# Kernel optimization log

Measured on AMD Instinct MI355X. Metric: run time of the kernel, lower is better.

## Reference

```python
import jax, jax.numpy as jnp
import numpy as np

B, C, H, W = 16, 128, 64, 64
C_OUT = 256
N_BANDS = 4
KS = [3, 5, 7, 11]
BN_EPS = 1e-5


def setup_inputs() -> dict:
    key = jax.random.key(0)
    ks = jax.random.split(key, 16)
    inp = {
        'x': jax.random.normal(ks[0], (B, C, H, W), dtype=jnp.float32),
        'conv_w0': jax.random.normal(ks[1], (C, 1, 3), dtype=jnp.float32) * 0.2,
        'conv_w1': jax.random.normal(ks[2], (C, 1, 5), dtype=jnp.float32) * 0.2,
        'conv_w2': jax.random.normal(ks[3], (C, 1, 7), dtype=jnp.float32) * 0.2,
        'conv_w3': jax.random.normal(ks[4], (C, 1, 11), dtype=jnp.float32) * 0.2,
        'bn_gamma': jax.random.uniform(ks[5], (N_BANDS, C), dtype=jnp.float32, minval=0.5, maxval=1.5),
        'bn_beta': jax.random.normal(ks[6], (N_BANDS, C), dtype=jnp.float32) * 0.1,
        'bn_mean': jax.random.normal(ks[7], (N_BANDS, C), dtype=jnp.float32) * 0.1,
        'bn_var': jax.random.uniform(ks[8], (N_BANDS, C), dtype=jnp.float32, minval=0.5, maxval=1.5),
        'scale_weights': jnp.ones((N_BANDS,), dtype=jnp.float32),
        'alpha': jnp.float32(0.5),
        'proj_w': jax.random.normal(ks[9], (C_OUT, C * N_BANDS), dtype=jnp.float32) * 0.04,
        'proj_b': jax.random.normal(ks[10], (C_OUT,), dtype=jnp.float32) * 0.02,
    }
    return inp


def _dwconv1d(xc, w):
    # xc: [B, C, L], w: [C, 1, k] depthwise, 'same' padding for odd k
    k = w.shape[-1]
    return jax.lax.conv_general_dilated(
        xc, w, window_strides=(1,), padding=[(k // 2, k // 2)],
        feature_group_count=xc.shape[1], dimension_numbers=('NCH', 'OIH', 'NCH'))


def _forward(x, conv_w0, conv_w1, conv_w2, conv_w3, bn_gamma, bn_beta, bn_mean,
             bn_var, scale_weights, alpha, proj_w, proj_b):
    b, c, h, w = x.shape
    L = h * w
    xs = x.reshape(b, c, L)                      # [B, C, L] (== x.view.transpose.transpose)
    norm_w = jax.nn.softmax(scale_weights)       # [n_bands]

    # --- multi-scale depthwise conv branch: conv -> BN(eval) -> GELU -> scale ---
    conv_bands = []
    for i, cw in enumerate([conv_w0, conv_w1, conv_w2, conv_w3]):
        y = _dwconv1d(xs, cw)                    # [B, C, L]
        inv = jax.lax.rsqrt(bn_var[i] + BN_EPS)  # [C]
        y = (y - bn_mean[i][:, None]) * (inv * bn_gamma[i])[:, None] + bn_beta[i][:, None]
        y = jax.nn.gelu(y, approximate=False)    # exact erf GELU (torch default)
        conv_bands.append(y.transpose(0, 2, 1) * norm_w[i])  # [B, L, C]

    # --- frequency band branch (interpolate to size L is identity: conv keeps L) ---
    xt = xs.transpose(0, 2, 1)                   # [B, L, C]
    Xf = jnp.fft.rfft(xt, axis=1)                # [B, n_freqs, C]
    n_freqs = L // 2 + 1
    band_size = n_freqs // N_BANDS
    fidx = jnp.arange(n_freqs)
    alpha_s = jax.nn.sigmoid(alpha)
    fused = []
    for i in range(N_BANDS):
        start = i * band_size
        end = (i + 1) * band_size if i < N_BANDS - 1 else n_freqs
        mask = (fidx >= start) & (fidx < end)
        band = jnp.fft.irfft(jnp.where(mask[None, :, None], Xf, 0), n=L, axis=1)
        fused.append(alpha_s * conv_bands[i] + (1.0 - alpha_s) * band)

    cat = jnp.concatenate(fused, axis=-1)        # [B, L, n_bands*C]
    out = cat @ proj_w.T + proj_b                # [B, L, C_out]
    return out.transpose(0, 2, 1).reshape(b, -1, h, w)


def reference(x, conv_w0, conv_w1, conv_w2, conv_w3, bn_gamma, bn_beta, bn_mean,
              bn_var, scale_weights, alpha, proj_w, proj_b):
    return _forward(x, conv_w0, conv_w1, conv_w2, conv_w3, bn_gamma, bn_beta,
                    bn_mean, bn_var, scale_weights, alpha, proj_w, proj_b)
```

## Files before the change

### kernel.cpp

```cpp
#include <hip/hip_runtime.h>
#include <math.h>

constexpr int LEN = 4096;
constexpr int NTHREADS = 512;
constexpr int PELEM = LEN / NTHREADS;
constexpr float INVN = 1.0f / 4096.0f;
constexpr float RHALF = 0.70710678118654752440f;
constexpr float TWK = -1.5339807878856412e-3f;

typedef __attribute__((ext_vector_type(8))) short bf16x8;
typedef __attribute__((ext_vector_type(4))) float f32x4;

#define APHYS(I) ((I) + ((I) >> 5))
#define ZOFF 8

__device__ __forceinline__ unsigned short f2bf(float f) {
    unsigned u = __float_as_uint(f);
    unsigned r = (u + 0x7fffu + ((u >> 16) & 1u)) >> 16;
    return (unsigned short)r;
}

__device__ __forceinline__ int drev3(int t) {
    return ((t & 7) << 6) | (((t >> 3) & 7) << 3) | (t >> 6);
}

__device__ __forceinline__ void cmul(float ar, float ai, float br, float bi,
                                     float& cr, float& ci) {
    cr = ar * br - ai * bi;
    ci = ar * bi + ai * br;
}

__device__ __forceinline__ void dft8_fwd(float (&xr)[8], float (&xi)[8]) {
    float b0r = xr[0] + xr[4], b0i = xi[0] + xi[4];
    float b1r = xr[1] + xr[5], b1i = xi[1] + xi[5];
    float b2r = xr[2] + xr[6], b2i = xi[2] + xi[6];
    float b3r = xr[3] + xr[7], b3i = xi[3] + xi[7];
    float c0r = xr[0] - xr[4], c0i = xi[0] - xi[4];
    float c1r = xr[1] - xr[5], c1i = xi[1] - xi[5];
    float c2r = xr[2] - xr[6], c2i = xi[2] - xi[6];
    float c3r = xr[3] - xr[7], c3i = xi[3] - xi[7];
    float d1r = RHALF * (c1r + c1i), d1i = RHALF * (c1i - c1r);
    float d2r = c2i,               d2i = -c2r;
    float d3r = -RHALF * (c3r - c3i), d3i = -RHALF * (c3r + c3i);
    float t0r = b0r + b2r, t0i = b0i + b2i;
    float t1r = b0r - b2r, t1i = b0i - b2i;
    float t2r = b1r + b3r, t2i = b1i + b3i;
    float t3r = b1r - b3r, t3i = b1i - b3i;
    xr[0] = t0r + t2r; xi[0] = t0i + t2i;
    xr[2] = t1r + t3i; xi[2] = t1i - t3r;
    xr[4] = t0r - t2r; xi[4] = t0i - t2i;
    xr[6] = t1r - t3i; xi[6] = t1i + t3r;
    t0r = c0r + d2r; t0i = c0i + d2i;
    t1r = c0r - d2r; t1i = c0i - d2i;
    t2r = d1r + d3r; t2i = d1i + d3i;
    t3r = d1r - d3r; t3i = d1i - d3i;
    xr[1] = t0r + t2r; xi[1] = t0i + t2i;
    xr[3] = t1r + t3i; xi[3] = t1i - t3r;
    xr[5] = t0r - t2r; xi[5] = t0i - t2i;
    xr[7] = t1r - t3i; xi[7] = t1i + t3r;
}

__device__ __forceinline__ void dft8_inv(float (&xr)[8], float (&xi)[8]) {
    float b0r = xr[0] + xr[4], b0i = xi[0] + xi[4];
    float b1r = xr[1] + xr[5], b1i = xi[1] + xi[5];
    float b2r = xr[2] + xr[6], b2i = xi[2] + xi[6];
    float b3r = xr[3] + xr[7], b3i = xi[3] + xi[7];
    float c0r = xr[0] - xr[4], c0i = xi[0] - xi[4];
    float c1r = xr[1] - xr[5], c1i = xi[1] - xi[5];
    float c2r = xr[2] - xr[6], c2i = xi[2] - xi[6];
    float c3r = xr[3] - xr[7], c3i = xi[3] - xi[7];
    float d1r = RHALF * (c1r - c1i), d1i = RHALF * (c1r + c1i);
    float d2r = -c2i,              d2i = c2r;
    float d3r = -RHALF * (c3r + c3i), d3i = RHALF * (c3r - c3i);
    float t0r = b0r + b2r, t0i = b0i + b2i;
    float t1r = b0r - b2r, t1i = b0i - b2i;
    float t2r = b1r + b3r, t2i = b1i + b3i;
    float t3r = b1r - b3r, t3i = b1i - b3i;
    xr[0] = t0r + t2r; xi[0] = t0i + t2i;
    xr[2] = t1r - t3i; xi[2] = t1i + t3r;
    xr[4] = t0r - t2r; xi[4] = t0i - t2i;
    xr[6] = t1r + t3i; xi[6] = t1i - t3r;
    t0r = c0r + d2r; t0i = c0i + d2i;
    t1r = c0r - d2r; t1i = c0i - d2i;
    t2r = d1r + d3r; t2i = d1i + d3i;
    t3r = d1r - d3r; t3i = d1i - d3i;
    xr[1] = t0r + t2r; xi[1] = t0i + t2i;
    xr[3] = t1r - t3i; xi[3] = t1i + t3r;
    xr[5] = t0r - t2r; xi[5] = t0i - t2i;
    xr[7] = t1r + t3i; xi[7] = t1i - t3r;
}

template <bool CONJ>
__device__ __forceinline__ void twmul7(float (&xr)[8], float (&xi)[8], int k1) {
    float sv, cv;
    __sincosf(TWK * (float)k1, &sv, &cv);
    float w1r = cv;
    float w1i = CONJ ? -sv : sv;
    float w2r, w2i, w3r, w3i, w4r, w4i, w5r, w5i, w6r, w6i, w7r, w7i;
    cmul(w1r, w1i, w1r, w1i, w2r, w2i);
    cmul(w2r, w2i, w1r, w1i, w3r, w3i);
    cmul(w2r, w2i, w2r, w2i, w4r, w4i);
    cmul(w4r, w4i, w1r, w1i, w5r, w5i);
    cmul(w4r, w4i, w2r, w2i, w6r, w6i);
    cmul(w4r, w4i, w3r, w3i, w7r, w7i);
    float orr, oii;
    cmul(xr[1], xi[1], w1r, w1i, orr, oii); xr[1] = orr; xi[1] = oii;
    cmul(xr[2], xi[2], w2r, w2i, orr, oii); xr[2] = orr; xi[2] = oii;
    cmul(xr[3], xi[3], w3r, w3i, orr, oii); xr[3] = orr; xi[3] = oii;
    cmul(xr[4], xi[4], w4r, w4i, orr, oii); xr[4] = orr; xi[4] = oii;
    cmul(xr[5], xi[5], w5r, w5i, orr, oii); xr[5] = orr; xi[5] = oii;
    cmul(xr[6], xi[6], w6r, w6i, orr, oii); xr[6] = orr; xi[6] = oii;
    cmul(xr[7], xi[7], w7r, w7i, orr, oii); xr[7] = orr; xi[7] = oii;
}

__device__ void dif_head(float* __restrict__ ar, float* __restrict__ ai, int tid) {
#pragma unroll
    for (int s = 0; s < 3; ++s) {
        __syncthreads();
        const int eshift = 3 * (3 - s);
        const int E = 1 << eshift;
        int j = tid & (E - 1);
        int g = tid >> eshift;
        int base = (g << (eshift + 3)) + j;
        float xr[8], xi[8];
#pragma unroll
        for (int m = 0; m < 8; ++m) {
            int idx = APHYS(base + (m << eshift));
            xr[m] = ar[idx]; xi[m] = ai[idx];
        }
        dft8_fwd(xr, xi);
        twmul7<false>(xr, xi, j << (3 * s));
#pragma unroll
        for (int m = 0; m < 8; ++m) {
            int idx = APHYS(base + (m << eshift));
            ar[idx] = xr[m]; ai[idx] = xi[m];
        }
    }
}

__device__ void dit_tail(float* __restrict__ ar, float* __restrict__ ai, int tid) {
#pragma unroll
    for (int s = 1; s < 4; ++s) {
        __syncthreads();
        const int eshift = 3 * s;
        const int E = 1 << eshift;
        int j = tid & (E - 1);
        int g = tid >> eshift;
        int base = (g << (eshift + 3)) + j;
        float xr[8], xi[8];
#pragma unroll
        for (int m = 0; m < 8; ++m) {
            int idx = APHYS(base + (m << eshift));
            xr[m] = ar[idx]; xi[m] = ai[idx];
        }
        twmul7<true>(xr, xi, j << (3 * (3 - s)));
        dft8_inv(xr, xi);
#pragma unroll
        for (int m = 0; m < 8; ++m) {
            int idx = APHYS(base + (m << eshift));
            ar[idx] = xr[m]; ai[idx] = xi[m];
        }
    }
}

__global__ __launch_bounds__(512) void k_bands(
    const float* __restrict__ x,
    const float* __restrict__ cw0, const float* __restrict__ cw1,
    const float* __restrict__ cw2, const float* __restrict__ cw3,
    const float* __restrict__ bng, const float* __restrict__ bnb,
    const float* __restrict__ bnm, const float* __restrict__ bnv,
    const float* __restrict__ sw, const float* __restrict__ alp,
    unsigned int* __restrict__ Fu) {
    __shared__ float wr[4223], wi[4223];
    __shared__ unsigned zpk[LEN + 16];

    const int tid = threadIdx.x;
    const int pair = blockIdx.x;
    const int b = blockIdx.y;
    const int c0 = 2 * pair, c1 = c0 + 1;

    const float* xp0 = x + ((size_t)b * 128 + c0) * LEN;
    const float* xp1 = xp0 + LEN;
#pragma unroll
    for (int p = 0; p < PELEM; ++p) {
        int l = tid + NTHREADS * p;
        float a0 = xp0[l], a1 = xp1[l];
        zpk[ZOFF + l] = (unsigned)f2bf(a0) | ((unsigned)f2bf(a1) << 16);
        wr[APHYS(l)] = a0; wi[APHYS(l)] = a1;
    }
    if (tid < 8) {
        zpk[tid] = 0u;
        zpk[ZOFF + LEN + tid] = 0u;
    }

    dif_head(wr, wi, tid);
    float Zr[8], Zi[8];
    __syncthreads();
#pragma unroll
    for (int m = 0; m < 8; ++m) {
        int idx = APHYS(8 * tid + m);
        Zr[m] = wr[idx]; Zi[m] = wi[idx];
    }
    dft8_fwd(Zr, Zi);

    const int D = drev3(tid);
    const int BM[8]  = {0, 1, 2, 3, 3, 2, 1, 0};
    const int BM0[8] = {0, 1, 2, 3, 3, 3, 2, 1};

    float s0w = sw[0], s1w = sw[1], s2w = sw[2], s3w = sw[3];
    float mx = fmaxf(fmaxf(s0w, s1w), fmaxf(s2w, s3w));
    float e0 = expf(s0w - mx), e1 = expf(s1w - mx), e2 = expf(s2w - mx), e3 = expf(s3w - mx);
    float esum = e0 + e1 + e2 + e3;
    float nwv[4] = {e0 / esum, e1 / esum, e2 / esum, e3 / esum};
    float alpha_s = 1.0f / (1.0f + expf(-alp[0]));
    float omaI = (1.0f - alpha_s) * INVN;

    const float* cwp[4] = {cw0, cw1, cw2, cw3};
    const int kk4[4] = {3, 5, 7, 11};

    unsigned int* dst = Fu + (size_t)b * (512 * LEN / 2);
    const int n = tid & 15;

#pragma unroll
    for (int band = 0; band < 4; ++band) {
        {
            float xr[8], xi[8];
#pragma unroll
            for (int m = 0; m < 8; ++m) {
                int bb = (D != 0) ? BM[m] : BM0[m];
                bool keep = (bb == band);
                xr[m] = keep ? Zr[m] : 0.0f;
                xi[m] = keep ? Zi[m] : 0.0f;
            }
            dft8_inv(xr, xi);
            __syncthreads();
#pragma unroll
            for (int m = 0; m < 8; ++m) {
                int idx = APHYS(8 * tid + m);
                wr[idx] = xr[m]; wi[idx] = xi[m];
            }
            dit_tail(wr, wi, tid);
        }

        const float* cw = cwp[band];
        const int kk = kk4[band];
        const int kh = kk >> 1;
        float A0 = rsqrtf(bnv[band * 128 + c0] + 1e-5f) * bng[band * 128 + c0];
        float B0 = bnb[band * 128 + c0] - bnm[band * 128 + c0] * A0;
        float A1 = rsqrtf(bnv[band * 128 + c1] + 1e-5f) * bng[band * 128 + c1];
        float B1 = bnb[band * 128 + c1] - bnm[band * 128 + c1] * A1;
        float nww = nwv[band];
#pragma unroll
        for (int p = 0; p < PELEM; ++p) {
            int l = tid + NTHREADS * p;
            float bvr = wr[APHYS(l)];
            float bvi = wi[APHYS(l)];
            float s0 = 0.f, s1 = 0.f;
#pragma unroll
            for (int q = 0; q < 11; ++q) {
                if (q < kk) {
                    unsigned uv = zpk[ZOFF + l + q - kh];
                    s0 += __uint_as_float(uv << 16) * cw[c0 * kk + q];
                    s1 += __uint_as_float(uv & 0xffff0000u) * cw[c1 * kk + q];
                }
            }
            float y0 = s0 * A0 + B0;
            y0 = 0.5f * y0 * (1.0f + erff(y0 * RHALF)) * nww;
            float y1 = s1 * A1 + B1;
            y1 = 0.5f * y1 * (1.0f + erff(y1 * RHALF)) * nww;
            float f0 = alpha_s * y0 + omaI * bvr;
            float f1 = alpha_s * y1 + omaI * bvi;
            int lb = (tid >> 4) + 32 * p;
            unsigned int val = (unsigned int)f2bf(f0) | ((unsigned int)f2bf(f1) << 16);
            dst[((lb * 64 + pair) * 16 + n) * 4 + band] = val;
        }
    }
}

__global__ void k_prep(const float* __restrict__ pw, unsigned short* __restrict__ Wq) {
    int idx = blockIdx.x * 256 + threadIdx.x;
    int o = idx >> 9, c = idx & 511;
    int band = c >> 7, pair = (c & 127) >> 1, lo = c & 1;
    int dstidx = (((o >> 4) * 64 + pair) * 16 + (o & 15)) * 8 + 2 * band + lo;
    Wq[dstidx] = f2bf(pw[idx]);
}

__global__ __launch_bounds__(256) void k_gemm(
    const unsigned short* __restrict__ Wq, const unsigned short* __restrict__ Fq,
    const float* __restrict__ pb, float* __restrict__ out) {
    const int tid = threadIdx.x;
    const int wave = tid >> 6, lane = tid & 63;
    const int h = lane >> 4, n16 = lane & 15;
    const int lt = blockIdx.x, b = blockIdx.y;
    const unsigned short* Fb = Fq + (size_t)b * 2097152;

    f32x4 acc[4][4];
#pragma unroll
    for (int mi = 0; mi < 4; ++mi)
#pragma unroll
        for (int ni = 0; ni < 4; ++ni) acc[mi][ni] = (f32x4){0.f, 0.f, 0.f, 0.f};

#pragma unroll
    for (int ks = 0; ks < 16; ++ks) {
        bf16x8 af[4], bfr[4];
#pragma unroll
        for (int mi = 0; mi < 4; ++mi) {
            int mb = wave * 4 + mi;
            af[mi] = *(const bf16x8*)(Wq + ((((mb * 64) + 4 * ks + h) * 16 + n16) << 3));
        }
#pragma unroll
        for (int ni = 0; ni < 4; ++ni) {
            int lb = lt * 4 + ni;
            bfr[ni] = *(const bf16x8*)(Fb + ((((lb * 64) + 4 * ks + h) * 16 + n16) << 3));
        }
#pragma unroll
        for (int mi = 0; mi < 4; ++mi)
#pragma unroll
            for (int ni = 0; ni < 4; ++ni)
                acc[mi][ni] = __builtin_amdgcn_mfma_f32_16x16x32_bf16(
                    af[mi], bfr[ni], acc[mi][ni], 0, 0, 0);
    }

#pragma unroll
    for (int mi = 0; mi < 4; ++mi) {
#pragma unroll
        for (int r = 0; r < 4; ++r) {
            int o = wave * 64 + mi * 16 + h * 4 + r;
            float bias = pb[o];
#pragma unroll
            for (int ni = 0; ni < 4; ++ni) {
                int l = lt * 64 + ni * 16 + n16;
                out[((size_t)(b * 256 + o)) * LEN + l] = acc[mi][ni][r] + bias;
            }
        }
    }
}

extern "C" void kernel_launch(void* const* d_in, const int* in_sizes, int n_in,
                              void* d_out, int out_size, void* d_ws, size_t ws_size,
                              hipStream_t stream) {
    const float* x   = (const float*)d_in[0];
    const float* cw0 = (const float*)d_in[1];
    const float* cw1 = (const float*)d_in[2];
    const float* cw2 = (const float*)d_in[3];
    const float* cw3 = (const float*)d_in[4];
    const float* bng = (const float*)d_in[5];
    const float* bnb = (const float*)d_in[6];
    const float* bnm = (const float*)d_in[7];
    const float* bnv = (const float*)d_in[8];
    const float* sw  = (const float*)d_in[9];
    const float* alp = (const float*)d_in[10];
    const float* pw  = (const float*)d_in[11];
    const float* pb  = (const float*)d_in[12];
    float* out = (float*)d_out;

    unsigned short* Wq = (unsigned short*)d_ws;
    unsigned int* Fu = (unsigned int*)((char*)d_ws + 262144);

    k_prep<<<512, 256, 0, stream>>>(pw, Wq);

    const size_t perB = (size_t)512 * LEN * 2;
    int chunk = (int)((ws_size > 262144 ? ws_size - 262144 : 0) / perB);
    if (chunk < 1) chunk = 1;
    if (chunk > 16) chunk = 16;

    for (int b0 = 0; b0 < 16; b0 += chunk) {
        int nb = 16 - b0 < chunk ? 16 - b0 : chunk;
        dim3 g1(64, nb);
        k_bands<<<g1, NTHREADS, 0, stream>>>(
            x + (size_t)b0 * 128 * LEN, cw0, cw1, cw2, cw3,
            bng, bnb, bnm, bnv, sw, alp, Fu);
        dim3 g2(64, nb);
        k_gemm<<<g2, 256, 0, stream>>>(
            Wq, (const unsigned short*)Fu, pb, out + (size_t)b0 * 256 * LEN);
    }
}
```

Baseline: 145.9 us.

## Fuse FFT first/last radix stages into registers and derive last band by subtraction

The first DIF radix-8 stage now runs directly on the values loaded from global memory, and the last DIT stage of each inverse transform stays in registers. This removes one shared-memory round trip and one barrier per transform. The fourth frequency band's inverse FFT is skipped and computed as the input minus the sum of the other three bands, since the band masks partition the spectrum. The conv input is now kept in fp32 shared arrays instead of packed bf16, which raises LDS use and may lower occupancy, but improves precision.

```diff
diff --git a/kernel.cpp b/kernel.cpp
--- a/kernel.cpp
+++ b/kernel.cpp
@@ -113,9 +113,9 @@
     cmul(xr[7], xi[7], w7r, w7i, orr, oii); xr[7] = orr; xi[7] = oii;
 }
 
-__device__ void dif_head(float* __restrict__ ar, float* __restrict__ ai, int tid) {
-#pragma unroll
-    for (int s = 0; s < 3; ++s) {
+__device__ void dif_mid(float* __restrict__ ar, float* __restrict__ ai, int tid) {
+#pragma unroll
+    for (int s = 1; s < 3; ++s) {
         __syncthreads();
         const int eshift = 3 * (3 - s);
         const int E = 1 << eshift;
@@ -138,9 +138,9 @@
     }
 }
 
-__device__ void dit_tail(float* __restrict__ ar, float* __restrict__ ai, int tid) {
-#pragma unroll
-    for (int s = 1; s < 4; ++s) {
+__device__ void dit_mid(float* __restrict__ ar, float* __restrict__ ai, int tid) {
+#pragma unroll
+    for (int s = 1; s < 3; ++s) {
         __syncthreads();
         const int eshift = 3 * s;
         const int E = 1 << eshift;
@@ -171,8 +171,8 @@
     const float* __restrict__ bnm, const float* __restrict__ bnv,
     const float* __restrict__ sw, const float* __restrict__ alp,
     unsigned int* __restrict__ Fu) {
+    __shared__ float zr[LEN + 16], zi[LEN + 16];
     __shared__ float wr[4223], wi[4223];
-    __shared__ unsigned zpk[LEN + 16];
 
     const int tid = threadIdx.x;
     const int pair = blockIdx.x;
@@ -181,21 +181,31 @@
 
     const float* xp0 = x + ((size_t)b * 128 + c0) * LEN;
     const float* xp1 = xp0 + LEN;
+
+    float Ar[8], Ai[8];
 #pragma unroll
     for (int p = 0; p < PELEM; ++p) {
         int l = tid + NTHREADS * p;
         float a0 = xp0[l], a1 = xp1[l];
-        zpk[ZOFF + l] = (unsigned)f2bf(a0) | ((unsigned)f2bf(a1) << 16);
-        wr[APHYS(l)] = a0; wi[APHYS(l)] = a1;
+        zr[ZOFF + l] = a0; zi[ZOFF + l] = a1;
+        Ar[p] = a0; Ai[p] = a1;
     }
     if (tid < 8) {
-        zpk[tid] = 0u;
-        zpk[ZOFF + LEN + tid] = 0u;
-    }
-
-    dif_head(wr, wi, tid);
+        zr[tid] = 0.f; zi[tid] = 0.f;
+        zr[ZOFF + LEN + tid] = 0.f; zi[ZOFF + LEN + tid] = 0.f;
+    }
+
+    dft8_fwd(Ar, Ai);
+    twmul7<false>(Ar, Ai, tid);
+#pragma unroll
+    for (int m = 0; m < 8; ++m) {
+        int idx = APHYS(tid + (m << 9));
+        wr[idx] = Ar[m]; wi[idx] = Ai[m];
+    }
+    dif_mid(wr, wi, tid);
+
+    __syncthreads();
     float Zr[8], Zi[8];
-    __syncthreads();
 #pragma unroll
     for (int m = 0; m < 8; ++m) {
         int idx = APHYS(8 * tid + m);
@@ -213,17 +223,22 @@
     float esum = e0 + e1 + e2 + e3;
     float nwv[4] = {e0 / esum, e1 / esum, e2 / esum, e3 / esum};
     float alpha_s = 1.0f / (1.0f + expf(-alp[0]));
-    float omaI = (1.0f - alpha_s) * INVN;
+    float oma = 1.0f - alpha_s;
 
     const float* cwp[4] = {cw0, cw1, cw2, cw3};
     const int kk4[4] = {3, 5, 7, 11};
 
+    float accr[PELEM], acci[PELEM];
+#pragma unroll
+    for (int p = 0; p < PELEM; ++p) { accr[p] = 0.f; acci[p] = 0.f; }
+
     unsigned int* dst = Fu + (size_t)b * (512 * LEN / 2);
     const int n = tid & 15;
 
 #pragma unroll
     for (int band = 0; band < 4; ++band) {
-        {
+        float bvr[8], bvi[8];
+        if (band < 3) {
             float xr[8], xi[8];
 #pragma unroll
             for (int m = 0; m < 8; ++m) {
@@ -239,7 +254,30 @@
                 int idx = APHYS(8 * tid + m);
                 wr[idx] = xr[m]; wi[idx] = xi[m];
             }
-            dit_tail(wr, wi, tid);
+            dit_mid(wr, wi, tid);
+
+            __syncthreads();
+#pragma unroll
+            for (int m = 0; m < 8; ++m) {
+                int idx = APHYS(tid + (m << 9));
+                xr[m] = wr[idx]; xi[m] = wi[idx];
+            }
+            twmul7<true>(xr, xi, tid);
+            dft8_inv(xr, xi);
+#pragma unroll
+            for (int m = 0; m < 8; ++m) {
+                bvr[m] = xr[m] * INVN;
+                bvi[m] = xi[m] * INVN;
+                accr[m] += bvr[m];
+                acci[m] += bvi[m];
+            }
+        } else {
+#pragma unroll
+            for (int p = 0; p < PELEM; ++p) {
+                int l = tid + NTHREADS * p;
+                bvr[p] = zr[ZOFF + l] - accr[p];
+                bvi[p] = zi[ZOFF + l] - acci[p];
+            }
         }
 
         const float* cw = cwp[band];
@@ -253,23 +291,21 @@
 #pragma unroll
         for (int p = 0; p < PELEM; ++p) {
             int l = tid + NTHREADS * p;
-            float bvr = wr[APHYS(l)];
-            float bvi = wi[APHYS(l)];
             float s0 = 0.f, s1 = 0.f;
 #pragma unroll
             for (int q = 0; q < 11; ++q) {
                 if (q < kk) {
-                    unsigned uv = zpk[ZOFF + l + q - kh];
-                    s0 += __uint_as_float(uv << 16) * cw[c0 * kk + q];
-                    s1 += __uint_as_float(uv & 0xffff0000u) * cw[c1 * kk + q];
+                    int idx = ZOFF + l + q - kh;
+                    s0 += zr[idx] * cw[c0 * kk + q];
+                    s1 += zi[idx] * cw[c1 * kk + q];
                 }
             }
             float y0 = s0 * A0 + B0;
             y0 = 0.5f * y0 * (1.0f + erff(y0 * RHALF)) * nww;
             float y1 = s1 * A1 + B1;
             y1 = 0.5f * y1 * (1.0f + erff(y1 * RHALF)) * nww;
-            float f0 = alpha_s * y0 + omaI * bvr;
-            float f1 = alpha_s * y1 + omaI * bvi;
+            float f0 = alpha_s * y0 + oma * bvr[p];
+            float f1 = alpha_s * y1 + oma * bvi[p];
             int lb = (tid >> 4) + 32 * p;
             unsigned int val = (unsigned int)f2bf(f0) | ((unsigned int)f2bf(f1) << 16);
             dst[((lb * 64 + pair) * 16 + n) * 4 + band] = val;
```

Result: faster. 136.2 us (-6.7%).
